# Kernel optimization log

Hardware: AMD Instinct MI355X
Metric: run time of the kernel (lower is better)

Reference implementation:

```python
import jax, jax.numpy as jnp
import numpy as np

EPS = 1e-5  # torch InstanceNorm3d default eps


def setup_inputs() -> dict:
    key = jax.random.key(0)
    ks = jax.random.split(key, 7)
    B, C, H, W, D = 2, 128, 48, 48, 48
    c_m, c_n = 128, 64
    return {
        "x": jax.random.normal(ks[0], (B, C, H, W, D), dtype=jnp.float32),
        "WA": jax.random.normal(ks[1], (c_m, C), dtype=jnp.float32) * (1.0 / np.sqrt(C)),
        "bA": jax.random.normal(ks[2], (c_m,), dtype=jnp.float32) * 0.01,
        "WB": jax.random.normal(ks[3], (c_n, C), dtype=jnp.float32) * (1.0 / np.sqrt(C)),
        "bB": jax.random.normal(ks[4], (c_n,), dtype=jnp.float32) * 0.01,
        "WV": jax.random.normal(ks[5], (c_n, C), dtype=jnp.float32) * (1.0 / np.sqrt(C)),
        "bV": jax.random.normal(ks[6], (c_n,), dtype=jnp.float32) * 0.01,
    }


def reference(x, WA, bA, WB, bB, WV, bV):
    B, C, H, W, D = x.shape
    L = H * W * D
    xf = x.reshape(B, C, L)
    # 1x1x1 Conv3d projections == per-voxel linear over channels
    A = jnp.einsum('bcl,mc->bml', xf, WA) + bA[None, :, None]   # (B, c_m, L)
    Bm = jnp.einsum('bcl,nc->bnl', xf, WB) + bB[None, :, None]  # (B, c_n, L)
    V = jnp.einsum('bcl,nc->bnl', xf, WV) + bV[None, :, None]   # (B, c_n, L)
    # attention maps: softmax over spatial positions
    attn_maps = jax.nn.softmax(Bm, axis=-1)                     # (B, c_n, L)
    # global descriptors: A @ attn_maps^T
    G = jnp.einsum('bml,bnl->bmn', A, attn_maps)                # (B, c_m, c_n)
    # attention vectors: softmax over c_n (channel) dim
    attn_vec = jax.nn.softmax(V, axis=1)                        # (B, c_n, L)
    Z = jnp.einsum('bmn,bnl->bml', G, attn_vec)                 # (B, c_m, L)
    # InstanceNorm3d (affine=False, biased variance) per (batch, channel)
    mean = jnp.mean(Z, axis=-1, keepdims=True)
    var = jnp.var(Z, axis=-1, keepdims=True)
    Zn = (Z - mean) * jax.lax.rsqrt(var + EPS)
    return Zn.reshape(B, Z.shape[1], H, W, D)
```

## Files before the change

### kernel.cpp

```cpp
#include <hip/hip_runtime.h>

#define LTOT 110592
#define EPSV 1e-5f

typedef _Float16 f16;
typedef __attribute__((ext_vector_type(4))) _Float16 f16x4;
typedef __attribute__((ext_vector_type(8))) _Float16 f16x8;
typedef __attribute__((ext_vector_type(4))) float f32x4;

#define MFMA16(a, b, c) __builtin_amdgcn_mfma_f32_16x16x32_f16(a, b, c, 0, 0, 0)

__device__ __forceinline__ f16x8 ld_w8(const float* p) {
  const float4 a = *(const float4*)p;
  const float4 b = *(const float4*)(p + 4);
  f16x8 f;
  f[0] = (f16)a.x; f[1] = (f16)a.y; f[2] = (f16)a.z; f[3] = (f16)a.w;
  f[4] = (f16)b.x; f[5] = (f16)b.y; f[6] = (f16)b.z; f[7] = (f16)b.w;
  return f;
}

__global__ __launch_bounds__(256, 2) void p1_proj_m(
    const float* __restrict__ x,
    const float* __restrict__ WB_, const float* __restrict__ bB_,
    const float* __restrict__ WV_, const float* __restrict__ bV_,
    f16* __restrict__ av_g, float* __restrict__ mpart, float* __restrict__ separt)
{
  __shared__ __align__(16) f16 XT[64 * 128];
  __shared__ __align__(16) f16 XC[128 * 64];
  __shared__ __align__(16) f16 EL[64 * 64];
  __shared__ __align__(16) f16 AVT[64 * 64];
  __shared__ float colp[4][64];
  const int tid = threadIdx.x, b = blockIdx.y, blk = blockIdx.x;
  const int ln = tid & 63, w = tid >> 6, g = ln >> 4;

  const int nB = w * 16 + (ln & 15);
  f16x8 wbf[4], wvf[4];
  #pragma unroll
  for (int ks = 0; ks < 4; ++ks) {
    wbf[ks] = ld_w8(&WB_[nB * 128 + ks * 32 + g * 8]);
    wvf[ks] = ld_w8(&WV_[nB * 128 + ks * 32 + g * 8]);
  }
  const float sB = bB_[nB];
  float biasV[4];
  #pragma unroll
  for (int r = 0; r < 4; ++r) biasV[r] = bV_[w * 16 + g * 4 + r];

  f32x4 macc[8];
  #pragma unroll
  for (int i = 0; i < 8; ++i) macc[i] = (f32x4){0.f, 0.f, 0.f, 0.f};
  float se = 0.f;

  const int xt_co = tid & 15, xt_lq = tid >> 4;
  const int xc_lo = tid & 7,  xc_c4 = tid >> 3;
  const size_t xb = (size_t)b * 128 * LTOT;

  for (int t = 0; t < 4; ++t) {
    const int l0 = (blk * 4 + t) * 64;
    __syncthreads();
    {
      float4 xr[8];
      #pragma unroll
      for (int j = 0; j < 8; ++j)
        xr[j] = *(const float4*)&x[xb + (size_t)(xt_co * 8 + j) * LTOT + l0 + xt_lq * 4];
      #pragma unroll
      for (int i = 0; i < 4; ++i) {
        const int l = xt_lq * 4 + i;
        f16x8 v;
        #pragma unroll
        for (int j = 0; j < 8; ++j) v[j] = (f16)(((const float*)&xr[j])[i]);
        *(f16x8*)&XT[l * 128 + ((xt_co * 8) ^ ((l & 7) << 3))] = v;
      }
    }
    #pragma unroll
    for (int i = 0; i < 4; ++i) {
      const int c = xc_c4 * 4 + i;
      const float4 a = *(const float4*)&x[xb + (size_t)c * LTOT + l0 + xc_lo * 8];
      const float4 d = *(const float4*)&x[xb + (size_t)c * LTOT + l0 + xc_lo * 8 + 4];
      f16x8 v;
      v[0] = (f16)a.x; v[1] = (f16)a.y; v[2] = (f16)a.z; v[3] = (f16)a.w;
      v[4] = (f16)d.x; v[5] = (f16)d.y; v[6] = (f16)d.z; v[7] = (f16)d.w;
      *(f16x8*)&XC[c * 64 + ((xc_lo * 8) ^ ((c & 7) << 3))] = v;
    }
    __syncthreads();
    f32x4 aB[4], aV[4];
    #pragma unroll
    for (int lt = 0; lt < 4; ++lt) {
      aB[lt] = (f32x4){0.f, 0.f, 0.f, 0.f};
      aV[lt] = (f32x4){0.f, 0.f, 0.f, 0.f};
      const int l = lt * 16 + (ln & 15);
      #pragma unroll
      for (int ks = 0; ks < 4; ++ks) {
        const f16x8 xf = *(const f16x8*)&XT[l * 128 + (((ks * 4 + g) * 8) ^ ((l & 7) << 3))];
        aB[lt] = MFMA16(xf, wbf[ks], aB[lt]);
        aV[lt] = MFMA16(wvf[ks], xf, aV[lt]);
      }
    }
    #pragma unroll
    for (int lt = 0; lt < 4; ++lt) {
      f16x4 ev4;
      #pragma unroll
      for (int r = 0; r < 4; ++r) {
        const float e = __expf(aB[lt][r] + sB);
        se += e;
        ev4[r] = (f16)e;
      }
      const int lq = lt * 16 + g * 4;
      *(f16x4*)&EL[nB * 64 + (lq ^ ((nB & 7) << 3))] = ev4;
    }
    float cs[4];
    #pragma unroll
    for (int ct = 0; ct < 4; ++ct) {
      f16x4 av4;
      float s = 0.f;
      #pragma unroll
      for (int r = 0; r < 4; ++r) {
        const float e = __expf(aV[ct][r] + biasV[r]);
        s += e;
        av4[r] = (f16)e;
      }
      cs[ct] = s;
      const int l = ct * 16 + (ln & 15);
      *(f16x4*)&AVT[l * 64 + ((w * 16 + g * 4) ^ ((l & 7) << 3))] = av4;
    }
    #pragma unroll
    for (int ct = 0; ct < 4; ++ct) {
      cs[ct] += __shfl_xor(cs[ct], 16);
      cs[ct] += __shfl_xor(cs[ct], 32);
    }
    {
      const float v = (g == 0) ? cs[0] : (g == 1) ? cs[1] : (g == 2) ? cs[2] : cs[3];
      colp[w][g * 16 + (ln & 15)] = v;
    }
    __syncthreads();
    {
      const int l = tid >> 2, q = tid & 3;
      const float rs = 1.f / (colp[0][l] + colp[1][l] + colp[2][l] + colp[3][l]);
      f16x8 a0 = *(const f16x8*)&AVT[l * 64 + ((q * 16) ^ ((l & 7) << 3))];
      f16x8 a1 = *(const f16x8*)&AVT[l * 64 + ((q * 16 + 8) ^ ((l & 7) << 3))];
      #pragma unroll
      for (int j = 0; j < 8; ++j) {
        a0[j] = (f16)((float)a0[j] * rs);
        a1[j] = (f16)((float)a1[j] * rs);
      }
      f16* gp = av_g + ((size_t)b * LTOT + l0 + l) * 64 + q * 16;
      *(f16x8*)&gp[0] = a0;
      *(f16x8*)&gp[8] = a1;
    }
    {
      f16x8 el[2];
      #pragma unroll
      for (int ks = 0; ks < 2; ++ks)
        el[ks] = *(const f16x8*)&EL[nB * 64 + ((ks * 32 + g * 8) ^ ((nB & 7) << 3))];
      #pragma unroll
      for (int cblk = 0; cblk < 8; ++cblk) {
        const int c = cblk * 16 + (ln & 15);
        #pragma unroll
        for (int ks = 0; ks < 2; ++ks) {
          const f16x8 xcf = *(const f16x8*)&XC[c * 64 + ((ks * 32 + g * 8) ^ ((c & 7) << 3))];
          macc[cblk] = MFMA16(el[ks], xcf, macc[cblk]);
        }
      }
    }
  }
  float* mp = mpart + (size_t)(b * 432 + blk) * 8192;
  #pragma unroll
  for (int cblk = 0; cblk < 8; ++cblk)
    #pragma unroll
    for (int r = 0; r < 4; ++r)
      mp[(w * 16 + g * 4 + r) * 128 + cblk * 16 + (ln & 15)] = macc[cblk][r];
  se += __shfl_xor(se, 16);
  se += __shfl_xor(se, 32);
  if (ln < 16) separt[(size_t)(b * 432 + blk) * 64 + w * 16 + ln] = se;
}

__global__ void p2a(const float* __restrict__ mpart, const float* __restrict__ separt,
                    float* __restrict__ mpart2, float* __restrict__ sesum)
{
  const int b = blockIdx.y, bx = blockIdx.x, tid = threadIdx.x;
  if (bx < 256) {
    const int seg = bx >> 5, chunk = bx & 31;
    const int idx = chunk * 256 + tid;
    float s = 0.f;
    for (int j = 0; j < 54; ++j)
      s += mpart[(size_t)(b * 432 + seg * 54 + j) * 8192 + idx];
    mpart2[(size_t)(b * 8 + seg) * 8192 + idx] = s;
  } else if (tid < 64) {
    float s = 0.f;
    for (int k = 0; k < 432; ++k) s += separt[(size_t)(b * 432 + k) * 64 + tid];
    sesum[b * 64 + tid] = s;
  }
}

__global__ void p2a2(const float* __restrict__ mpart2, float* __restrict__ msum)
{
  const int b = blockIdx.y;
  const int idx = blockIdx.x * 256 + threadIdx.x;
  float s = 0.f;
  #pragma unroll
  for (int k = 0; k < 8; ++k) s += mpart2[(size_t)(b * 8 + k) * 8192 + idx];
  msum[(size_t)b * 8192 + idx] = s;
}

__global__ void p2b(const float* __restrict__ WA_, const float* __restrict__ bA_,
                    const float* __restrict__ msum, const float* __restrict__ sesum,
                    float* __restrict__ g32, f16* __restrict__ g16)
{
  const int b = blockIdx.y;
  const int idx = blockIdx.x * 256 + threadIdx.x;
  const int m = idx >> 6, n = idx & 63;
  float s = 0.f;
  #pragma unroll 4
  for (int c = 0; c < 128; ++c) s += WA_[m * 128 + c] * msum[(size_t)b * 8192 + n * 128 + c];
  const float gv = s / sesum[b * 64 + n] + bA_[m];
  g32[(size_t)b * 8192 + m * 64 + n] = gv;
  g16[(size_t)b * 8192 + m * 64 + (n ^ ((m & 7) << 3))] = (f16)gv;
}

__global__ __launch_bounds__(256, 2) void p3_cov(
    const f16* __restrict__ av_g, float* __restrict__ cpart, float* __restrict__ mupart)
{
  __shared__ __align__(16) f16 AV[64 * 64];
  const int tid = threadIdx.x, b = blockIdx.y, blk = blockIdx.x;
  const int ln = tid & 63, w = tid >> 6, g = ln >> 4;
  const int nq4 = (tid & 15) * 4, lq4 = (tid >> 4) * 4;
  const int nmu = tid >> 2, qmu = tid & 3;

  f32x4 cacc[4];
  #pragma unroll
  for (int j = 0; j < 4; ++j) cacc[j] = (f32x4){0.f, 0.f, 0.f, 0.f};
  float muacc = 0.f;

  for (int t = 0; t < 8; ++t) {
    const int l0 = (blk * 8 + t) * 64;
    __syncthreads();
    {
      f16x4 rd[4];
      #pragma unroll
      for (int i = 0; i < 4; ++i)
        rd[i] = *(const f16x4*)&av_g[((size_t)b * LTOT + l0 + lq4 + i) * 64 + nq4];
      #pragma unroll
      for (int j = 0; j < 4; ++j) {
        const int n = nq4 + j;
        f16x4 wr;
        #pragma unroll
        for (int i = 0; i < 4; ++i) wr[i] = rd[i][j];
        *(f16x4*)&AV[n * 64 + (lq4 ^ ((n & 7) << 3))] = wr;
      }
    }
    __syncthreads();
    {
      const f16x8 a0 = *(const f16x8*)&AV[nmu * 64 + ((qmu * 16) ^ ((nmu & 7) << 3))];
      const f16x8 a1 = *(const f16x8*)&AV[nmu * 64 + ((qmu * 16 + 8) ^ ((nmu & 7) << 3))];
      #pragma unroll
      for (int j = 0; j < 8; ++j) muacc += (float)a0[j] + (float)a1[j];
    }
    const int nA = w * 16 + (ln & 15);
    f16x8 caf[2];
    #pragma unroll
    for (int ks = 0; ks < 2; ++ks)
      caf[ks] = *(const f16x8*)&AV[nA * 64 + ((ks * 32 + g * 8) ^ ((nA & 7) << 3))];
    #pragma unroll
    for (int nct = 0; nct < 4; ++nct) {
      const int nb = nct * 16 + (ln & 15);
      #pragma unroll
      for (int ks = 0; ks < 2; ++ks) {
        const f16x8 cbf = *(const f16x8*)&AV[nb * 64 + ((ks * 32 + g * 8) ^ ((nb & 7) << 3))];
        cacc[nct] = MFMA16(caf[ks], cbf, cacc[nct]);
      }
    }
  }
  float* cp = cpart + (size_t)(b * 216 + blk) * 4096;
  #pragma unroll
  for (int nct = 0; nct < 4; ++nct)
    #pragma unroll
    for (int r = 0; r < 4; ++r)
      cp[(w * 16 + g * 4 + r) * 64 + nct * 16 + (ln & 15)] = cacc[nct][r];
  muacc += __shfl_xor(muacc, 1);
  muacc += __shfl_xor(muacc, 2);
  if (qmu == 0) mupart[(size_t)(b * 216 + blk) * 64 + nmu] = muacc;
}

__global__ void p4a(const float* __restrict__ cpart, const float* __restrict__ mupart,
                    float* __restrict__ csum, float* __restrict__ musum)
{
  const int b = blockIdx.y, bx = blockIdx.x, tid = threadIdx.x;
  if (bx < 64) {
    const int idx = bx * 64 + (tid >> 2), q = tid & 3;
    float s = 0.f;
    for (int k = q; k < 216; k += 4) s += cpart[(size_t)(b * 216 + k) * 4096 + idx];
    s += __shfl_xor(s, 1);
    s += __shfl_xor(s, 2);
    if (q == 0) csum[(size_t)b * 4096 + idx] = s;
  } else if (tid < 64) {
    float s = 0.f;
    for (int k = 0; k < 216; ++k) s += mupart[(size_t)(b * 216 + k) * 64 + tid];
    musum[b * 64 + tid] = s;
  }
}

__global__ void p4b(const float* __restrict__ csum, const float* __restrict__ musum,
                    const float* __restrict__ g32, float* __restrict__ mr)
{
  __shared__ __align__(16) float CL[4096];
  __shared__ __align__(16) float GLs[32 * 68];
  __shared__ float MUL[64];
  const int tid = threadIdx.x, b = blockIdx.y, bx = blockIdx.x;
  #pragma unroll
  for (int k = 0; k < 16; ++k) CL[k * 256 + tid] = csum[(size_t)b * 4096 + k * 256 + tid];
  #pragma unroll
  for (int k = 0; k < 8; ++k) {
    const int idx = k * 256 + tid;
    const int m_ = idx >> 6, n_ = idx & 63;
    GLs[m_ * 68 + n_] = g32[(size_t)b * 8192 + (bx * 32 + m_) * 64 + n_];
  }
  if (tid < 64) MUL[tid] = musum[b * 64 + tid];
  __syncthreads();
  const int mrow = (tid >> 3) * 68, oct = tid & 7;
  float q = 0.f;
  #pragma unroll
  for (int q4 = 0; q4 < 2; ++q4) {
    const int npb = oct * 8 + q4 * 4;
    float t0 = 0.f, t1 = 0.f, t2 = 0.f, t3 = 0.f;
    #pragma unroll 8
    for (int n = 0; n < 64; ++n) {
      const float4 cv = *(const float4*)&CL[n * 64 + npb];
      const float gv = GLs[mrow + n];
      t0 += gv * cv.x; t1 += gv * cv.y; t2 += gv * cv.z; t3 += gv * cv.w;
    }
    const float4 gq = *(const float4*)&GLs[mrow + npb];
    q += t0 * gq.x + t1 * gq.y + t2 * gq.z + t3 * gq.w;
  }
  q += __shfl_xor(q, 1); q += __shfl_xor(q, 2); q += __shfl_xor(q, 4);
  if (oct == 0) {
    float meanq = 0.f;
    #pragma unroll 8
    for (int n = 0; n < 64; ++n) meanq += GLs[mrow + n] * MUL[n];
    const int m = bx * 32 + (tid >> 3);
    const float mean = meanq / (float)LTOT;
    const float var = fmaxf(q / (float)LTOT - mean * mean, 0.f);
    mr[(b * 128 + m) * 2] = mean;
    mr[(b * 128 + m) * 2 + 1] = rsqrtf(var + EPSV);
  }
}

__global__ __launch_bounds__(256, 2) void p5_z(
    const f16* __restrict__ av_g, const f16* __restrict__ g16,
    const float* __restrict__ mr, float* __restrict__ out)
{
  __shared__ __align__(16) f16 AVT[64 * 64];
  const int tid = threadIdx.x, b = blockIdx.y, blk = blockIdx.x;
  const int ln = tid & 63, w = tid >> 6, g = ln >> 4;
  const int lst = tid & 63, pst = tid >> 6;

  f16x8 gf[2][2];
  float mean_[2][4], rsig_[2][4];
  #pragma unroll
  for (int mct = 0; mct < 2; ++mct) {
    const int mA = w * 32 + mct * 16 + (ln & 15);
    #pragma unroll
    for (int ks = 0; ks < 2; ++ks)
      gf[mct][ks] = *(const f16x8*)&g16[(size_t)b * 8192 + mA * 64 +
                                        (((ks * 4 + g) * 8) ^ ((mA & 7) << 3))];
    #pragma unroll
    for (int r = 0; r < 4; ++r) {
      const int m = w * 32 + mct * 16 + g * 4 + r;
      mean_[mct][r] = mr[(b * 128 + m) * 2];
      rsig_[mct][r] = mr[(b * 128 + m) * 2 + 1];
    }
  }

  for (int t = 0; t < 4; ++t) {
    const int l0 = (blk * 4 + t) * 64;
    __syncthreads();
    {
      const f16* gp = av_g + ((size_t)b * LTOT + l0 + lst) * 64 + pst * 16;
      const f16x8 a0 = *(const f16x8*)&gp[0];
      const f16x8 a1 = *(const f16x8*)&gp[8];
      *(f16x8*)&AVT[lst * 64 + ((pst * 16) ^ ((lst & 7) << 3))] = a0;
      *(f16x8*)&AVT[lst * 64 + ((pst * 16 + 8) ^ ((lst & 7) << 3))] = a1;
    }
    __syncthreads();
    #pragma unroll
    for (int lt = 0; lt < 4; ++lt) {
      const int l = lt * 16 + (ln & 15);
      f16x8 avf[2];
      #pragma unroll
      for (int ks = 0; ks < 2; ++ks)
        avf[ks] = *(const f16x8*)&AVT[l * 64 + (((ks * 4 + g) * 8) ^ ((l & 7) << 3))];
      #pragma unroll
      for (int mct = 0; mct < 2; ++mct) {
        f32x4 z = {0.f, 0.f, 0.f, 0.f};
        #pragma unroll
        for (int ks = 0; ks < 2; ++ks) z = MFMA16(gf[mct][ks], avf[ks], z);
        #pragma unroll
        for (int r = 0; r < 4; ++r) {
          const int m = w * 32 + mct * 16 + g * 4 + r;
          out[(size_t)(b * 128 + m) * LTOT + l0 + l] =
              (z[r] - mean_[mct][r]) * rsig_[mct][r];
        }
      }
    }
  }
}

extern "C" void kernel_launch(void* const* d_in, const int* in_sizes, int n_in,
                              void* d_out, int out_size, void* d_ws, size_t ws_size,
                              hipStream_t stream)
{
  const float* x  = (const float*)d_in[0];
  const float* WA = (const float*)d_in[1];
  const float* bA = (const float*)d_in[2];
  const float* WB = (const float*)d_in[3];
  const float* bB = (const float*)d_in[4];
  const float* WV = (const float*)d_in[5];
  const float* bV = (const float*)d_in[6];
  float* out = (float*)d_out;

  float* w = (float*)d_ws;
  float* mpart  = w;
  float* mpart2 = mpart + 7077888;
  float* separt = mpart2 + 131072;
  float* msum   = separt + 55296;
  float* sesum  = msum + 16384;
  float* g32    = sesum + 128;
  f16*   g16f   = (f16*)(g32 + 16384);
  f16*   av_g   = g16f + 16384;
  float* cpart  = (float*)(av_g + 14155776);
  float* mupart = cpart + 1769472;
  float* csum   = mupart + 27648;
  float* musum  = csum + 8192;
  float* mr     = musum + 128;

  p1_proj_m<<<dim3(432, 2), 256, 0, stream>>>(x, WB, bB, WV, bV, av_g, mpart, separt);
  p2a<<<dim3(257, 2), 256, 0, stream>>>(mpart, separt, mpart2, sesum);
  p2a2<<<dim3(32, 2), 256, 0, stream>>>(mpart2, msum);
  p2b<<<dim3(32, 2), 256, 0, stream>>>(WA, bA, msum, sesum, g32, g16f);
  p3_cov<<<dim3(216, 2), 256, 0, stream>>>(av_g, cpart, mupart);
  p4a<<<dim3(65, 2), 256, 0, stream>>>(cpart, mupart, csum, musum);
  p4b<<<dim3(4, 2), 256, 0, stream>>>(csum, musum, g32, mr);
  p5_z<<<dim3(432, 2), 256, 0, stream>>>(av_g, g16f, mr, out);
}
```

Measured before the change: 137.8 us.

## Merge reduction kernels, prefetch tiles across iterations, and reload x once in projection

The projection kernel now loads each x tile once into registers and builds both LDS layouts from it, where before it read x twice. It also prefetches the next tile while the current one is being computed. p3_cov and p5_z gain the same register prefetch; p3_cov runs twice as many blocks with fewer iterations each. The separate reduction kernels are folded into one red_all kernel, and the G computation and norm statistics are folded into p4g, cutting the launch count from eight to five. Launch bounds are raised for occupancy, which may cause register spills, and the cov partial buffer doubles in size.

```diff
diff --git a/kernel.cpp b/kernel.cpp
--- a/kernel.cpp
+++ b/kernel.cpp
@@ -19,7 +19,7 @@
   return f;
 }
 
-__global__ __launch_bounds__(256, 2) void p1_proj_m(
+__global__ __launch_bounds__(256, 3) void p1_proj_m(
     const float* __restrict__ x,
     const float* __restrict__ WB_, const float* __restrict__ bB_,
     const float* __restrict__ WV_, const float* __restrict__ bV_,
@@ -50,38 +50,43 @@
   for (int i = 0; i < 8; ++i) macc[i] = (f32x4){0.f, 0.f, 0.f, 0.f};
   float se = 0.f;
 
-  const int xt_co = tid & 15, xt_lq = tid >> 4;
-  const int xc_lo = tid & 7,  xc_c4 = tid >> 3;
+  const int co = tid & 15, lq = tid >> 4;
   const size_t xb = (size_t)b * 128 * LTOT;
+
+  float4 xr[8];
+  {
+    const int l0 = blk * 256;
+    #pragma unroll
+    for (int j = 0; j < 8; ++j)
+      xr[j] = *(const float4*)&x[xb + (size_t)(co * 8 + j) * LTOT + l0 + lq * 4];
+  }
 
   for (int t = 0; t < 4; ++t) {
     const int l0 = (blk * 4 + t) * 64;
     __syncthreads();
-    {
-      float4 xr[8];
+    #pragma unroll
+    for (int i = 0; i < 4; ++i) {
+      const int l = lq * 4 + i;
+      f16x8 v;
+      #pragma unroll
+      for (int j = 0; j < 8; ++j) v[j] = (f16)(((const float*)&xr[j])[i]);
+      *(f16x8*)&XT[l * 128 + ((co * 8) ^ ((l & 7) << 3))] = v;
+    }
+    #pragma unroll
+    for (int j = 0; j < 8; ++j) {
+      const int c = co * 8 + j;
+      f16x4 q;
+      q[0] = (f16)xr[j].x; q[1] = (f16)xr[j].y;
+      q[2] = (f16)xr[j].z; q[3] = (f16)xr[j].w;
+      *(f16x4*)&XC[c * 64 + ((lq * 4) ^ ((c & 7) << 3))] = q;
+    }
+    __syncthreads();
+    if (t < 3) {
+      const int l0n = l0 + 64;
       #pragma unroll
       for (int j = 0; j < 8; ++j)
-        xr[j] = *(const float4*)&x[xb + (size_t)(xt_co * 8 + j) * LTOT + l0 + xt_lq * 4];
-      #pragma unroll
-      for (int i = 0; i < 4; ++i) {
-        const int l = xt_lq * 4 + i;
-        f16x8 v;
-        #pragma unroll
-        for (int j = 0; j < 8; ++j) v[j] = (f16)(((const float*)&xr[j])[i]);
-        *(f16x8*)&XT[l * 128 + ((xt_co * 8) ^ ((l & 7) << 3))] = v;
-      }
-    }
-    #pragma unroll
-    for (int i = 0; i < 4; ++i) {
-      const int c = xc_c4 * 4 + i;
-      const float4 a = *(const float4*)&x[xb + (size_t)c * LTOT + l0 + xc_lo * 8];
-      const float4 d = *(const float4*)&x[xb + (size_t)c * LTOT + l0 + xc_lo * 8 + 4];
-      f16x8 v;
-      v[0] = (f16)a.x; v[1] = (f16)a.y; v[2] = (f16)a.z; v[3] = (f16)a.w;
-      v[4] = (f16)d.x; v[5] = (f16)d.y; v[6] = (f16)d.z; v[7] = (f16)d.w;
-      *(f16x8*)&XC[c * 64 + ((xc_lo * 8) ^ ((c & 7) << 3))] = v;
-    }
-    __syncthreads();
+        xr[j] = *(const float4*)&x[xb + (size_t)(co * 8 + j) * LTOT + l0n + lq * 4];
+    }
     f32x4 aB[4], aV[4];
     #pragma unroll
     for (int lt = 0; lt < 4; ++lt) {
@@ -104,8 +109,8 @@
         se += e;
         ev4[r] = (f16)e;
       }
-      const int lq = lt * 16 + g * 4;
-      *(f16x4*)&EL[nB * 64 + (lq ^ ((nB & 7) << 3))] = ev4;
+      const int lql = lt * 16 + g * 4;
+      *(f16x4*)&EL[nB * 64 + (lql ^ ((nB & 7) << 3))] = ev4;
     }
     float cs[4];
     #pragma unroll
@@ -173,50 +178,7 @@
   if (ln < 16) separt[(size_t)(b * 432 + blk) * 64 + w * 16 + ln] = se;
 }
 
-__global__ void p2a(const float* __restrict__ mpart, const float* __restrict__ separt,
-                    float* __restrict__ mpart2, float* __restrict__ sesum)
-{
-  const int b = blockIdx.y, bx = blockIdx.x, tid = threadIdx.x;
-  if (bx < 256) {
-    const int seg = bx >> 5, chunk = bx & 31;
-    const int idx = chunk * 256 + tid;
-    float s = 0.f;
-    for (int j = 0; j < 54; ++j)
-      s += mpart[(size_t)(b * 432 + seg * 54 + j) * 8192 + idx];
-    mpart2[(size_t)(b * 8 + seg) * 8192 + idx] = s;
-  } else if (tid < 64) {
-    float s = 0.f;
-    for (int k = 0; k < 432; ++k) s += separt[(size_t)(b * 432 + k) * 64 + tid];
-    sesum[b * 64 + tid] = s;
-  }
-}
-
-__global__ void p2a2(const float* __restrict__ mpart2, float* __restrict__ msum)
-{
-  const int b = blockIdx.y;
-  const int idx = blockIdx.x * 256 + threadIdx.x;
-  float s = 0.f;
-  #pragma unroll
-  for (int k = 0; k < 8; ++k) s += mpart2[(size_t)(b * 8 + k) * 8192 + idx];
-  msum[(size_t)b * 8192 + idx] = s;
-}
-
-__global__ void p2b(const float* __restrict__ WA_, const float* __restrict__ bA_,
-                    const float* __restrict__ msum, const float* __restrict__ sesum,
-                    float* __restrict__ g32, f16* __restrict__ g16)
-{
-  const int b = blockIdx.y;
-  const int idx = blockIdx.x * 256 + threadIdx.x;
-  const int m = idx >> 6, n = idx & 63;
-  float s = 0.f;
-  #pragma unroll 4
-  for (int c = 0; c < 128; ++c) s += WA_[m * 128 + c] * msum[(size_t)b * 8192 + n * 128 + c];
-  const float gv = s / sesum[b * 64 + n] + bA_[m];
-  g32[(size_t)b * 8192 + m * 64 + n] = gv;
-  g16[(size_t)b * 8192 + m * 64 + (n ^ ((m & 7) << 3))] = (f16)gv;
-}
-
-__global__ __launch_bounds__(256, 2) void p3_cov(
+__global__ __launch_bounds__(256, 4) void p3_cov(
     const f16* __restrict__ av_g, float* __restrict__ cpart, float* __restrict__ mupart)
 {
   __shared__ __align__(16) f16 AV[64 * 64];
@@ -230,14 +192,14 @@
   for (int j = 0; j < 4; ++j) cacc[j] = (f32x4){0.f, 0.f, 0.f, 0.f};
   float muacc = 0.f;
 
-  for (int t = 0; t < 8; ++t) {
-    const int l0 = (blk * 8 + t) * 64;
+  f16x4 rd[4];
+  #pragma unroll
+  for (int i = 0; i < 4; ++i)
+    rd[i] = *(const f16x4*)&av_g[((size_t)b * LTOT + blk * 256 + lq4 + i) * 64 + nq4];
+
+  for (int t = 0; t < 4; ++t) {
     __syncthreads();
     {
-      f16x4 rd[4];
-      #pragma unroll
-      for (int i = 0; i < 4; ++i)
-        rd[i] = *(const f16x4*)&av_g[((size_t)b * LTOT + l0 + lq4 + i) * 64 + nq4];
       #pragma unroll
       for (int j = 0; j < 4; ++j) {
         const int n = nq4 + j;
@@ -248,6 +210,12 @@
       }
     }
     __syncthreads();
+    if (t < 3) {
+      const int l0n = (blk * 4 + t + 1) * 64;
+      #pragma unroll
+      for (int i = 0; i < 4; ++i)
+        rd[i] = *(const f16x4*)&av_g[((size_t)b * LTOT + l0n + lq4 + i) * 64 + nq4];
+    }
     {
       const f16x8 a0 = *(const f16x8*)&AV[nmu * 64 + ((qmu * 16) ^ ((nmu & 7) << 3))];
       const f16x8 a1 = *(const f16x8*)&AV[nmu * 64 + ((qmu * 16 + 8) ^ ((nmu & 7) << 3))];
@@ -269,7 +237,7 @@
       }
     }
   }
-  float* cp = cpart + (size_t)(b * 216 + blk) * 4096;
+  float* cp = cpart + (size_t)(b * 432 + blk) * 4096;
   #pragma unroll
   for (int nct = 0; nct < 4; ++nct)
     #pragma unroll
@@ -277,43 +245,89 @@
       cp[(w * 16 + g * 4 + r) * 64 + nct * 16 + (ln & 15)] = cacc[nct][r];
   muacc += __shfl_xor(muacc, 1);
   muacc += __shfl_xor(muacc, 2);
-  if (qmu == 0) mupart[(size_t)(b * 216 + blk) * 64 + nmu] = muacc;
-}
-
-__global__ void p4a(const float* __restrict__ cpart, const float* __restrict__ mupart,
-                    float* __restrict__ csum, float* __restrict__ musum)
+  if (qmu == 0) mupart[(size_t)(b * 432 + blk) * 64 + nmu] = muacc;
+}
+
+__global__ void red_all(const float* __restrict__ mpart, const float* __restrict__ separt,
+                        const float* __restrict__ cpart, const float* __restrict__ mupart,
+                        float* __restrict__ mpart2, float* __restrict__ sesum,
+                        float* __restrict__ csum, float* __restrict__ musum)
 {
   const int b = blockIdx.y, bx = blockIdx.x, tid = threadIdx.x;
-  if (bx < 64) {
-    const int idx = bx * 64 + (tid >> 2), q = tid & 3;
+  if (bx < 256) {
+    const int seg = bx >> 5, chunk = bx & 31;
+    const int idx = chunk * 256 + tid;
     float s = 0.f;
-    for (int k = q; k < 216; k += 4) s += cpart[(size_t)(b * 216 + k) * 4096 + idx];
-    s += __shfl_xor(s, 1);
-    s += __shfl_xor(s, 2);
-    if (q == 0) csum[(size_t)b * 4096 + idx] = s;
-  } else if (tid < 64) {
+    #pragma unroll 4
+    for (int j = 0; j < 54; ++j)
+      s += mpart[(size_t)(b * 432 + seg * 54 + j) * 8192 + idx];
+    mpart2[(size_t)(b * 8 + seg) * 8192 + idx] = s;
+  } else if (bx < 272) {
+    const int idx = (bx - 256) * 256 + tid;
     float s = 0.f;
-    for (int k = 0; k < 216; ++k) s += mupart[(size_t)(b * 216 + k) * 64 + tid];
-    musum[b * 64 + tid] = s;
-  }
-}
-
-__global__ void p4b(const float* __restrict__ csum, const float* __restrict__ musum,
-                    const float* __restrict__ g32, float* __restrict__ mr)
-{
+    #pragma unroll 4
+    for (int k = 0; k < 432; ++k)
+      s += cpart[(size_t)(b * 432 + k) * 4096 + idx];
+    csum[(size_t)b * 4096 + idx] = s;
+  } else {
+    if (tid < 64) {
+      float s = 0.f;
+      #pragma unroll 4
+      for (int k = 0; k < 432; ++k) s += separt[(size_t)(b * 432 + k) * 64 + tid];
+      sesum[b * 64 + tid] = s;
+    } else if (tid < 128) {
+      const int n = tid - 64;
+      float s = 0.f;
+      #pragma unroll 4
+      for (int k = 0; k < 432; ++k) s += mupart[(size_t)(b * 432 + k) * 64 + n];
+      musum[b * 64 + n] = s;
+    }
+  }
+}
+
+__global__ __launch_bounds__(256, 1) void p4g(
+    const float* __restrict__ mpart2, const float* __restrict__ sesum,
+    const float* __restrict__ csum, const float* __restrict__ musum,
+    const float* __restrict__ WA_, const float* __restrict__ bA_,
+    f16* __restrict__ g16, float* __restrict__ mr)
+{
+  __shared__ __align__(16) float MS[8192];
+  __shared__ __align__(16) float WAs[32 * 129];
   __shared__ __align__(16) float CL[4096];
-  __shared__ __align__(16) float GLs[32 * 68];
+  __shared__ __align__(16) float GR[32 * 68];
+  __shared__ float SE[64];
   __shared__ float MUL[64];
   const int tid = threadIdx.x, b = blockIdx.y, bx = blockIdx.x;
-  #pragma unroll
-  for (int k = 0; k < 16; ++k) CL[k * 256 + tid] = csum[(size_t)b * 4096 + k * 256 + tid];
-  #pragma unroll
-  for (int k = 0; k < 8; ++k) {
-    const int idx = k * 256 + tid;
-    const int m_ = idx >> 6, n_ = idx & 63;
-    GLs[m_ * 68 + n_] = g32[(size_t)b * 8192 + (bx * 32 + m_) * 64 + n_];
-  }
-  if (tid < 64) MUL[tid] = musum[b * 64 + tid];
+
+  for (int it = 0; it < 32; ++it) {
+    const int i = it * 256 + tid;
+    float s = 0.f;
+    #pragma unroll
+    for (int k = 0; k < 8; ++k) s += mpart2[(size_t)(b * 8 + k) * 8192 + i];
+    MS[i] = s;
+  }
+  for (int it = 0; it < 16; ++it) {
+    const int i = it * 256 + tid;
+    WAs[(i >> 7) * 129 + (i & 127)] = WA_[(bx * 32 + (i >> 7)) * 128 + (i & 127)];
+  }
+  for (int it = 0; it < 16; ++it)
+    CL[it * 256 + tid] = csum[(size_t)b * 4096 + it * 256 + tid];
+  if (tid < 64) {
+    SE[tid] = sesum[b * 64 + tid];
+    MUL[tid] = musum[b * 64 + tid];
+  }
+  __syncthreads();
+  for (int it = 0; it < 8; ++it) {
+    const int e = it * 256 + tid;
+    const int n = e >> 5, ml = e & 31;
+    float s = 0.f;
+    #pragma unroll 4
+    for (int c = 0; c < 128; ++c) s += WAs[ml * 129 + c] * MS[n * 128 + c];
+    const int m = bx * 32 + ml;
+    const float gv = s / SE[n] + bA_[m];
+    GR[ml * 68 + n] = gv;
+    g16[(size_t)b * 8192 + m * 64 + (n ^ ((m & 7) << 3))] = (f16)gv;
+  }
   __syncthreads();
   const int mrow = (tid >> 3) * 68, oct = tid & 7;
   float q = 0.f;
@@ -324,17 +338,17 @@
     #pragma unroll 8
     for (int n = 0; n < 64; ++n) {
       const float4 cv = *(const float4*)&CL[n * 64 + npb];
-      const float gv = GLs[mrow + n];
+      const float gv = GR[mrow + n];
       t0 += gv * cv.x; t1 += gv * cv.y; t2 += gv * cv.z; t3 += gv * cv.w;
     }
-    const float4 gq = *(const float4*)&GLs[mrow + npb];
+    const float4 gq = *(const float4*)&GR[mrow + npb];
     q += t0 * gq.x + t1 * gq.y + t2 * gq.z + t3 * gq.w;
   }
   q += __shfl_xor(q, 1); q += __shfl_xor(q, 2); q += __shfl_xor(q, 4);
   if (oct == 0) {
     float meanq = 0.f;
     #pragma unroll 8
-    for (int n = 0; n < 64; ++n) meanq += GLs[mrow + n] * MUL[n];
+    for (int n = 0; n < 64; ++n) meanq += GR[mrow + n] * MUL[n];
     const int m = bx * 32 + (tid >> 3);
     const float mean = meanq / (float)LTOT;
     const float var = fmaxf(q / (float)LTOT - mean * mean, 0.f);
@@ -343,7 +357,7 @@
   }
 }
 
-__global__ __launch_bounds__(256, 2) void p5_z(
+__global__ __launch_bounds__(256, 3) void p5_z(
     const f16* __restrict__ av_g, const f16* __restrict__ g16,
     const float* __restrict__ mr, float* __restrict__ out)
 {
@@ -369,17 +383,24 @@
     }
   }
 
+  f16x8 pa0, pa1;
+  {
+    const f16* gp = av_g + ((size_t)b * LTOT + blk * 256 + lst) * 64 + pst * 16;
+    pa0 = *(const f16x8*)&gp[0];
+    pa1 = *(const f16x8*)&gp[8];
+  }
+
   for (int t = 0; t < 4; ++t) {
     const int l0 = (blk * 4 + t) * 64;
     __syncthreads();
-    {
-      const f16* gp = av_g + ((size_t)b * LTOT + l0 + lst) * 64 + pst * 16;
-      const f16x8 a0 = *(const f16x8*)&gp[0];
-      const f16x8 a1 = *(const f16x8*)&gp[8];
-      *(f16x8*)&AVT[lst * 64 + ((pst * 16) ^ ((lst & 7) << 3))] = a0;
-      *(f16x8*)&AVT[lst * 64 + ((pst * 16 + 8) ^ ((lst & 7) << 3))] = a1;
-    }
-    __syncthreads();
+    *(f16x8*)&AVT[lst * 64 + ((pst * 16) ^ ((lst & 7) << 3))] = pa0;
+    *(f16x8*)&AVT[lst * 64 + ((pst * 16 + 8) ^ ((lst & 7) << 3))] = pa1;
+    __syncthreads();
+    if (t < 3) {
+      const f16* gp = av_g + ((size_t)b * LTOT + l0 + 64 + lst) * 64 + pst * 16;
+      pa0 = *(const f16x8*)&gp[0];
+      pa1 = *(const f16x8*)&gp[8];
+    }
     #pragma unroll
     for (int lt = 0; lt < 4; ++lt) {
       const int l = lt * 16 + (ln & 15);
@@ -420,23 +441,19 @@
   float* mpart  = w;
   float* mpart2 = mpart + 7077888;
   float* separt = mpart2 + 131072;
-  float* msum   = separt + 55296;
-  float* sesum  = msum + 16384;
-  float* g32    = sesum + 128;
-  f16*   g16f   = (f16*)(g32 + 16384);
+  float* sesum  = separt + 55296;
+  f16*   g16f   = (f16*)(sesum + 128);
   f16*   av_g   = g16f + 16384;
   float* cpart  = (float*)(av_g + 14155776);
-  float* mupart = cpart + 1769472;
-  float* csum   = mupart + 27648;
+  float* mupart = cpart + 3538944;
+  float* csum   = mupart + 55296;
   float* musum  = csum + 8192;
   float* mr     = musum + 128;
 
   p1_proj_m<<<dim3(432, 2), 256, 0, stream>>>(x, WB, bB, WV, bV, av_g, mpart, separt);
-  p2a<<<dim3(257, 2), 256, 0, stream>>>(mpart, separt, mpart2, sesum);
-  p2a2<<<dim3(32, 2), 256, 0, stream>>>(mpart2, msum);
-  p2b<<<dim3(32, 2), 256, 0, stream>>>(WA, bA, msum, sesum, g32, g16f);
-  p3_cov<<<dim3(216, 2), 256, 0, stream>>>(av_g, cpart, mupart);
-  p4a<<<dim3(65, 2), 256, 0, stream>>>(cpart, mupart, csum, musum);
-  p4b<<<dim3(4, 2), 256, 0, stream>>>(csum, musum, g32, mr);
+  p3_cov<<<dim3(432, 2), 256, 0, stream>>>(av_g, cpart, mupart);
+  red_all<<<dim3(273, 2), 256, 0, stream>>>(mpart, separt, cpart, mupart,
+                                            mpart2, sesum, csum, musum);
+  p4g<<<dim3(4, 2), 256, 0, stream>>>(mpart2, sesum, csum, musum, WA, bA, g16f, mr);
   p5_z<<<dim3(432, 2), 256, 0, stream>>>(av_g, g16f, mr, out);
 }
```

After: 171.5 us. 1.24x slower.
